# Kernel tuning notes

Hardware: AMD Instinct MI355X
Metric: run time of the kernel (lower is better)

Reference implementation:

```python
import jax, jax.numpy as jnp
import numpy as np

OUT_GRID = (256, 256)  # output_grid_shape


def setup_inputs() -> dict:
    key = jax.random.key(0)
    k1, k2 = jax.random.split(key)
    N, H, W, C = 16, 256, 256, 32
    x = jax.random.normal(k1, (N, H, W, C), dtype=jnp.float32)
    # loc network: global mean pool -> dense(6); small weights + identity-affine bias
    W_loc = jax.random.normal(k2, (C, 6), dtype=jnp.float32) * 0.01
    b_loc = jnp.array([1.0, 0.0, 0.0, 0.0, 1.0, 0.0], dtype=jnp.float32)
    return {"x": x, "W_loc": W_loc, "b_loc": b_loc}


def _spatial_transform(x, W_loc, b_loc):
    N, H, W, C = x.shape
    Ho, Wo = OUT_GRID
    # loc_network: params (N, 6) -> theta (N, 2, 3)
    params = jnp.mean(x, axis=(1, 2)) @ W_loc + b_loc
    theta = params.reshape(N, 2, 3)
    # grid_transform_fn: affine on [-1,1]-normalized output index grid
    gy = jnp.linspace(-1.0, 1.0, Ho, dtype=jnp.float32)
    gx = jnp.linspace(-1.0, 1.0, Wo, dtype=jnp.float32)
    Gy, Gx = jnp.meshgrid(gy, gx, indexing="ij")
    grid = jnp.stack([Gy.ravel(), Gx.ravel(), jnp.ones(Ho * Wo, jnp.float32)], axis=0)  # (3, Ho*Wo)
    coords = jnp.einsum("npq,qm->npm", theta, grid).reshape(N, 2, Ho, Wo)  # in ~[-1,1]
    # interpolate_bilinear with clip (wrap=False)
    maxes = jnp.array([H - 1, W - 1], dtype=jnp.float32)
    up = (coords + 1.0) * maxes[None, :, None, None] * 0.5  # upscale to pixel coords
    f = jnp.floor(up)
    frac = up - f  # (N, 2, Ho, Wo)
    fi = f.astype(jnp.int32)
    batch = jnp.arange(N)[:, None, None]
    out = jnp.zeros((N, Ho, Wo, C), dtype=x.dtype)
    for by in (0, 1):  # 2^dim corner offsets (bitfield)
        for bx in (0, 1):
            cy = jnp.clip(fi[:, 0] + by, 0, H - 1)
            cx = jnp.clip(fi[:, 1] + bx, 0, W - 1)
            wy = frac[:, 0] if by else 1.0 - frac[:, 0]
            wx = frac[:, 1] if bx else 1.0 - frac[:, 1]
            out = out + x[batch, cy, cx] * (wy * wx)[..., None]
    return out


def reference(x, W_loc, b_loc):
    return _spatial_transform(x, W_loc, b_loc)
```

## Files before the change

kernel.cpp:

```cpp
#include <hip/hip_runtime.h>


#define NIMG 16
#define HDIM 256
#define WDIM 256
#define CH   32
#define HW   (HDIM * WDIM)
#define BPI  64

typedef float f32x4 __attribute__((ext_vector_type(4)));

__global__ __launch_bounds__(256) void st_sum_kernel(
    const float* __restrict__ x, float* __restrict__ partials) {
    const int n   = blockIdx.x >> 6;
    const int blk = blockIdx.x & (BPI - 1);
    const int tid = threadIdx.x;
    const int cg  = tid & 7;
    const int sp  = tid >> 3;

    const float4* xp = (const float4*)(x + (size_t)n * HW * CH);
    float4 a0 = make_float4(0.f, 0.f, 0.f, 0.f);
    float4 a1 = make_float4(0.f, 0.f, 0.f, 0.f);
    float4 a2 = make_float4(0.f, 0.f, 0.f, 0.f);
    float4 a3 = make_float4(0.f, 0.f, 0.f, 0.f);
    int s = blk * 32 + sp;
    #pragma unroll
    for (int it = 0; it < 8; ++it) {
        float4 v0 = xp[(size_t)(s       ) * 8 + cg];
        float4 v1 = xp[(size_t)(s + 2048) * 8 + cg];
        float4 v2 = xp[(size_t)(s + 4096) * 8 + cg];
        float4 v3 = xp[(size_t)(s + 6144) * 8 + cg];
        a0.x += v0.x; a0.y += v0.y; a0.z += v0.z; a0.w += v0.w;
        a1.x += v1.x; a1.y += v1.y; a1.z += v1.z; a1.w += v1.w;
        a2.x += v2.x; a2.y += v2.y; a2.z += v2.z; a2.w += v2.w;
        a3.x += v3.x; a3.y += v3.y; a3.z += v3.z; a3.w += v3.w;
        s += 8192;
    }
    a0.x += a1.x; a0.y += a1.y; a0.z += a1.z; a0.w += a1.w;
    a2.x += a3.x; a2.y += a3.y; a2.z += a3.z; a2.w += a3.w;
    a0.x += a2.x; a0.y += a2.y; a0.z += a2.z; a0.w += a2.w;

    __shared__ float4 red[256];
    red[tid] = a0;
    __syncthreads();
    for (int stride = 16; stride >= 1; stride >>= 1) {
        if (sp < stride) {
            float4 o = red[(sp + stride) * 8 + cg];
            a0.x += o.x; a0.y += o.y; a0.z += o.z; a0.w += o.w;
            red[tid] = a0;
        }
        __syncthreads();
    }
    if (sp == 0) {
        ((float4*)(partials + ((size_t)blk * NIMG + n) * CH))[cg] = a0;
    }
}

__global__ __launch_bounds__(256) void st_interp_kernel(
    const float* __restrict__ x, const float* __restrict__ partials,
    const float* __restrict__ W_loc, const float* __restrict__ b_loc,
    float* __restrict__ out) {
    const int bid = (int)blockIdx.x;
    const int swz = (bid & 7) * 1024 + (bid >> 3);
    const int n   = swz >> 9;
    const int r   = swz & 511;
    const int tid = threadIdx.x;

    __shared__ float red2[8][CH];
    __shared__ float th_s[8];
    {
        const int c = tid & 31, g = tid >> 5;
        float s = 0.f;
        #pragma unroll
        for (int j = 0; j < 8; ++j)
            s += partials[(size_t)((g * 8 + j) * NIMG + n) * CH + c];
        red2[g][c] = s;
        __syncthreads();
        if (g == 0) {
            float m = 0.f;
            #pragma unroll
            for (int j = 0; j < 8; ++j) m += red2[j][c];
            red2[0][c] = m * (1.0f / (float)HW);
        }
        __syncthreads();
        if (tid < 6) {
            float acc = b_loc[tid];
            for (int c2 = 0; c2 < CH; ++c2)
                acc = fmaf(red2[0][c2], W_loc[c2 * 6 + tid], acc);
            th_s[tid] = acc;
        }
        __syncthreads();
    }
    const float t00 = th_s[0], t01 = th_s[1], t02 = th_s[2];
    const float t10 = th_s[3], t11 = th_s[4], t12 = th_s[5];

    const int ty = r >> 3;
    const int tx = r & 7;
    const int p  = tid >> 3;
    const int cg = tid & 7;

    const int ho = ty * 4 + (p >> 3);
    const float gy = fmaf((float)ho, 2.0f / 255.0f, -1.0f);
    const float cy = fmaf(t00, gy, t02);
    const float cx = fmaf(t10, gy, t12);

    const float4* xp = (const float4*)(x + (size_t)n * HW * CH);

    int   off0[4], off1[4], off2[4], off3[4];
    float w00[4], w01[4], w10[4], w11[4];
    int   wo[4];
    #pragma unroll
    for (int k = 0; k < 4; ++k) {
        wo[k] = tx * 32 + (p & 7) + k * 8;
        const float gx = fmaf((float)wo[k], 2.0f / 255.0f, -1.0f);
        const float uy = (fmaf(t01, gx, cy) + 1.0f) * 127.5f;
        const float ux = (fmaf(t11, gx, cx) + 1.0f) * 127.5f;
        const float fy = floorf(uy), fx = floorf(ux);
        const float ry = uy - fy, rx = ux - fx;
        const int iy0 = min(max((int)fy,     0), HDIM - 1);
        const int iy1 = min(max((int)fy + 1, 0), HDIM - 1);
        const int ix0 = min(max((int)fx,     0), WDIM - 1);
        const int ix1 = min(max((int)fx + 1, 0), WDIM - 1);
        off0[k] = (iy0 * WDIM + ix0) * 8;
        off1[k] = (iy0 * WDIM + ix1) * 8;
        off2[k] = (iy1 * WDIM + ix0) * 8;
        off3[k] = (iy1 * WDIM + ix1) * 8;
        w00[k] = (1.0f - ry) * (1.0f - rx);
        w01[k] = (1.0f - ry) * rx;
        w10[k] = ry * (1.0f - rx);
        w11[k] = ry * rx;
    }

    float4 v00[4], v01[4], v10[4], v11[4];
    #pragma unroll
    for (int k = 0; k < 4; ++k) {
        v00[k] = xp[(size_t)off0[k] + cg];
        v01[k] = xp[(size_t)off1[k] + cg];
        v10[k] = xp[(size_t)off2[k] + cg];
        v11[k] = xp[(size_t)off3[k] + cg];
    }

    f32x4* op = (f32x4*)(out + (size_t)n * HW * CH);
    #pragma unroll
    for (int k = 0; k < 4; ++k) {
        f32x4 o;
        o.x = v00[k].x * w00[k] + v01[k].x * w01[k] + v10[k].x * w10[k] + v11[k].x * w11[k];
        o.y = v00[k].y * w00[k] + v01[k].y * w01[k] + v10[k].y * w10[k] + v11[k].y * w11[k];
        o.z = v00[k].z * w00[k] + v01[k].z * w01[k] + v10[k].z * w10[k] + v11[k].z * w11[k];
        o.w = v00[k].w * w00[k] + v01[k].w * w01[k] + v10[k].w * w10[k] + v11[k].w * w11[k];
        __builtin_nontemporal_store(o, &op[(size_t)(ho * WDIM + wo[k]) * 8 + cg]);
    }
}

extern "C" void kernel_launch(void* const* d_in, const int* in_sizes, int n_in,
                              void* d_out, int out_size, void* d_ws, size_t ws_size,
                              hipStream_t stream) {
    const float* x     = (const float*)d_in[0];
    const float* W_loc = (const float*)d_in[1];
    const float* b_loc = (const float*)d_in[2];
    float* out = (float*)d_out;

    float* partials = (float*)d_ws;

    st_sum_kernel<<<NIMG * BPI, 256, 0, stream>>>(x, partials);
    st_interp_kernel<<<NIMG * (HW / 128), 256, 0, stream>>>(
        x, partials, W_loc, b_loc, out);
}
```

Baseline: 63.03 us.

## Stage bilinear source footprint in LDS per 8x32 output tile

The interpolation kernel now covers an 8x32 output tile per block instead of 4x32, which halves the grid. Each block computes the bounding box of its source footprint from the tile corners and, if that box fits within 384 pixels, copies it cooperatively into shared memory. The four corner gathers are then served from LDS rather than from scattered global loads, with a global-gather fallback when the box does not fit. The cost is 48KB of LDS per block, which lowers occupancy, plus an extra barrier and a serial row-by-row staging loop.

New measurement: 75.60 us. 1.2x slower.

```diff
diff --git a/kernel.cpp b/kernel.cpp
--- a/kernel.cpp
+++ b/kernel.cpp
@@ -7,6 +7,7 @@
 #define CH   32
 #define HW   (HDIM * WDIM)
 #define BPI  64
+#define STAGE_PX 384
 
 typedef float f32x4 __attribute__((ext_vector_type(4)));
 
@@ -61,13 +62,15 @@
     const float* __restrict__ W_loc, const float* __restrict__ b_loc,
     float* __restrict__ out) {
     const int bid = (int)blockIdx.x;
-    const int swz = (bid & 7) * 1024 + (bid >> 3);
-    const int n   = swz >> 9;
-    const int r   = swz & 511;
+    const int swz = (bid & 7) * 512 + (bid >> 3);
+    const int n   = swz >> 8;
+    const int r   = swz & 255;
     const int tid = threadIdx.x;
 
-    __shared__ float red2[8][CH];
-    __shared__ float th_s[8];
+    __shared__ float  red2[8][CH];
+    __shared__ float  th_s[8];
+    __shared__ float4 stage[STAGE_PX * 8];
+
     {
         const int c = tid & 31, g = tid >> 5;
         float s = 0.f;
@@ -94,61 +97,110 @@
     const float t00 = th_s[0], t01 = th_s[1], t02 = th_s[2];
     const float t10 = th_s[3], t11 = th_s[4], t12 = th_s[5];
 
-    const int ty = r >> 3;
-    const int tx = r & 7;
+    const int ty = r >> 3, tx = r & 7;
+    const int row0 = ty * 8, col0 = tx * 32;
     const int p  = tid >> 3;
     const int cg = tid & 7;
-
-    const int ho = ty * 4 + (p >> 3);
-    const float gy = fmaf((float)ho, 2.0f / 255.0f, -1.0f);
-    const float cy = fmaf(t00, gy, t02);
-    const float cx = fmaf(t10, gy, t12);
+    const int wo = col0 + p;
+
+    const float gx  = fmaf((float)wo, 2.0f / 255.0f, -1.0f);
+    const float ayx = fmaf(t01, gx, t02);
+    const float axx = fmaf(t11, gx, t12);
+
+    const float gyA = fmaf((float)row0,        2.0f / 255.0f, -1.0f);
+    const float gyB = fmaf((float)(row0 + 7),  2.0f / 255.0f, -1.0f);
+    const float gxA = fmaf((float)col0,        2.0f / 255.0f, -1.0f);
+    const float gxB = fmaf((float)(col0 + 31), 2.0f / 255.0f, -1.0f);
+    const float uy1 = (fmaf(t00, gyA, fmaf(t01, gxA, t02)) + 1.0f) * 127.5f;
+    const float uy2 = (fmaf(t00, gyA, fmaf(t01, gxB, t02)) + 1.0f) * 127.5f;
+    const float uy3 = (fmaf(t00, gyB, fmaf(t01, gxA, t02)) + 1.0f) * 127.5f;
+    const float uy4 = (fmaf(t00, gyB, fmaf(t01, gxB, t02)) + 1.0f) * 127.5f;
+    const float ux1 = (fmaf(t10, gyA, fmaf(t11, gxA, t12)) + 1.0f) * 127.5f;
+    const float ux2 = (fmaf(t10, gyA, fmaf(t11, gxB, t12)) + 1.0f) * 127.5f;
+    const float ux3 = (fmaf(t10, gyB, fmaf(t11, gxA, t12)) + 1.0f) * 127.5f;
+    const float ux4 = (fmaf(t10, gyB, fmaf(t11, gxB, t12)) + 1.0f) * 127.5f;
+    const float uymin = fminf(fminf(uy1, uy2), fminf(uy3, uy4));
+    const float uymax = fmaxf(fmaxf(uy1, uy2), fmaxf(uy3, uy4));
+    const float uxmin = fminf(fminf(ux1, ux2), fminf(ux3, ux4));
+    const float uxmax = fmaxf(fmaxf(ux1, ux2), fmaxf(ux3, ux4));
+    const int iy_lo = min(max((int)floorf(uymin),     0), HDIM - 1);
+    const int iy_hi = min(max((int)floorf(uymax) + 1, 0), HDIM - 1);
+    const int ix_lo = min(max((int)floorf(uxmin),     0), WDIM - 1);
+    const int ix_hi = min(max((int)floorf(uxmax) + 1, 0), WDIM - 1);
+    const int Rr = iy_hi - iy_lo + 1;
+    const int Cc = ix_hi - ix_lo + 1;
+    const bool finite = (uymin == uymin) && (uymax == uymax) &&
+                        (uxmin == uxmin) && (uxmax == uxmax);
+    const bool fits = finite && Rr >= 1 && Cc >= 1 && (Rr * Cc) <= STAGE_PX;
 
     const float4* xp = (const float4*)(x + (size_t)n * HW * CH);
-
-    int   off0[4], off1[4], off2[4], off3[4];
-    float w00[4], w01[4], w10[4], w11[4];
-    int   wo[4];
-    #pragma unroll
-    for (int k = 0; k < 4; ++k) {
-        wo[k] = tx * 32 + (p & 7) + k * 8;
-        const float gx = fmaf((float)wo[k], 2.0f / 255.0f, -1.0f);
-        const float uy = (fmaf(t01, gx, cy) + 1.0f) * 127.5f;
-        const float ux = (fmaf(t11, gx, cx) + 1.0f) * 127.5f;
-        const float fy = floorf(uy), fx = floorf(ux);
-        const float ry = uy - fy, rx = ux - fx;
-        const int iy0 = min(max((int)fy,     0), HDIM - 1);
-        const int iy1 = min(max((int)fy + 1, 0), HDIM - 1);
-        const int ix0 = min(max((int)fx,     0), WDIM - 1);
-        const int ix1 = min(max((int)fx + 1, 0), WDIM - 1);
-        off0[k] = (iy0 * WDIM + ix0) * 8;
-        off1[k] = (iy0 * WDIM + ix1) * 8;
-        off2[k] = (iy1 * WDIM + ix0) * 8;
-        off3[k] = (iy1 * WDIM + ix1) * 8;
-        w00[k] = (1.0f - ry) * (1.0f - rx);
-        w01[k] = (1.0f - ry) * rx;
-        w10[k] = ry * (1.0f - rx);
-        w11[k] = ry * rx;
-    }
-
-    float4 v00[4], v01[4], v10[4], v11[4];
-    #pragma unroll
-    for (int k = 0; k < 4; ++k) {
-        v00[k] = xp[(size_t)off0[k] + cg];
-        v01[k] = xp[(size_t)off1[k] + cg];
-        v10[k] = xp[(size_t)off2[k] + cg];
-        v11[k] = xp[(size_t)off3[k] + cg];
-    }
-
     f32x4* op = (f32x4*)(out + (size_t)n * HW * CH);
-    #pragma unroll
-    for (int k = 0; k < 4; ++k) {
-        f32x4 o;
-        o.x = v00[k].x * w00[k] + v01[k].x * w01[k] + v10[k].x * w10[k] + v11[k].x * w11[k];
-        o.y = v00[k].y * w00[k] + v01[k].y * w01[k] + v10[k].y * w10[k] + v11[k].y * w11[k];
-        o.z = v00[k].z * w00[k] + v01[k].z * w01[k] + v10[k].z * w10[k] + v11[k].z * w11[k];
-        o.w = v00[k].w * w00[k] + v01[k].w * w01[k] + v10[k].w * w10[k] + v11[k].w * w11[k];
-        __builtin_nontemporal_store(o, &op[(size_t)(ho * WDIM + wo[k]) * 8 + cg]);
+
+    if (fits) {
+        const int C8 = Cc * 8;
+        for (int rr = 0; rr < Rr; ++rr) {
+            const float4* src = xp + ((size_t)((iy_lo + rr) * WDIM + ix_lo)) * 8;
+            float4* dst = stage + rr * C8;
+            for (int u = tid; u < C8; u += 256) dst[u] = src[u];
+        }
+        __syncthreads();
+
+        #pragma unroll
+        for (int k = 0; k < 8; ++k) {
+            const int ho = row0 + k;
+            const float gy = fmaf((float)ho, 2.0f / 255.0f, -1.0f);
+            const float uy = (fmaf(t00, gy, ayx) + 1.0f) * 127.5f;
+            const float ux = (fmaf(t10, gy, axx) + 1.0f) * 127.5f;
+            const float fy = floorf(uy), fx = floorf(ux);
+            const float ry = uy - fy, rx = ux - fx;
+            const int iy0 = min(max((int)fy,     0), HDIM - 1);
+            const int iy1 = min(max((int)fy + 1, 0), HDIM - 1);
+            const int ix0 = min(max((int)fx,     0), WDIM - 1);
+            const int ix1 = min(max((int)fx + 1, 0), WDIM - 1);
+            const int ly0 = iy0 - iy_lo, ly1 = iy1 - iy_lo;
+            const int lx0 = ix0 - ix_lo, lx1 = ix1 - ix_lo;
+            float4 v00 = stage[(ly0 * Cc + lx0) * 8 + cg];
+            float4 v01 = stage[(ly0 * Cc + lx1) * 8 + cg];
+            float4 v10 = stage[(ly1 * Cc + lx0) * 8 + cg];
+            float4 v11 = stage[(ly1 * Cc + lx1) * 8 + cg];
+            const float w00 = (1.0f - ry) * (1.0f - rx);
+            const float w01 = (1.0f - ry) * rx;
+            const float w10 = ry * (1.0f - rx);
+            const float w11 = ry * rx;
+            f32x4 o;
+            o.x = v00.x * w00 + v01.x * w01 + v10.x * w10 + v11.x * w11;
+            o.y = v00.y * w00 + v01.y * w01 + v10.y * w10 + v11.y * w11;
+            o.z = v00.z * w00 + v01.z * w01 + v10.z * w10 + v11.z * w11;
+            o.w = v00.w * w00 + v01.w * w01 + v10.w * w10 + v11.w * w11;
+            __builtin_nontemporal_store(o, &op[(size_t)(ho * WDIM + wo) * 8 + cg]);
+        }
+    } else {
+        for (int k = 0; k < 8; ++k) {
+            const int ho = row0 + k;
+            const float gy = fmaf((float)ho, 2.0f / 255.0f, -1.0f);
+            const float uy = (fmaf(t00, gy, ayx) + 1.0f) * 127.5f;
+            const float ux = (fmaf(t10, gy, axx) + 1.0f) * 127.5f;
+            const float fy = floorf(uy), fx = floorf(ux);
+            const float ry = uy - fy, rx = ux - fx;
+            const int iy0 = min(max((int)fy,     0), HDIM - 1);
+            const int iy1 = min(max((int)fy + 1, 0), HDIM - 1);
+            const int ix0 = min(max((int)fx,     0), WDIM - 1);
+            const int ix1 = min(max((int)fx + 1, 0), WDIM - 1);
+            float4 v00 = xp[(size_t)(iy0 * WDIM + ix0) * 8 + cg];
+            float4 v01 = xp[(size_t)(iy0 * WDIM + ix1) * 8 + cg];
+            float4 v10 = xp[(size_t)(iy1 * WDIM + ix0) * 8 + cg];
+            float4 v11 = xp[(size_t)(iy1 * WDIM + ix1) * 8 + cg];
+            const float w00 = (1.0f - ry) * (1.0f - rx);
+            const float w01 = (1.0f - ry) * rx;
+            const float w10 = ry * (1.0f - rx);
+            const float w11 = ry * rx;
+            f32x4 o;
+            o.x = v00.x * w00 + v01.x * w01 + v10.x * w10 + v11.x * w11;
+            o.y = v00.y * w00 + v01.y * w01 + v10.y * w10 + v11.y * w11;
+            o.z = v00.z * w00 + v01.z * w01 + v10.z * w10 + v11.z * w11;
+            o.w = v00.w * w00 + v01.w * w01 + v10.w * w10 + v11.w * w11;
+            __builtin_nontemporal_store(o, &op[(size_t)(ho * WDIM + wo) * 8 + cg]);
+        }
     }
 }
 
@@ -163,6 +215,6 @@
     float* partials = (float*)d_ws;
 
     st_sum_kernel<<<NIMG * BPI, 256, 0, stream>>>(x, partials);
-    st_interp_kernel<<<NIMG * (HW / 128), 256, 0, stream>>>(
+    st_interp_kernel<<<NIMG * (HW / 256), 256, 0, stream>>>(
         x, partials, W_loc, b_loc, out);
 }
```

## Walk output rows per thread and reuse bottom-row corners as next top-row corners

Applied to the files above, without the earlier changes.

Each thread now produces 8 consecutive output rows at one column instead of 4 columns in one row. Because theta is near identity, the bottom corner pair of one row usually becomes the top pair of the next, so those two loads are skipped when the indices match. This roughly halves gather load instructions and halves the grid size. The cost is that loads now sit inside a serial dependent loop with a data-dependent branch, which may reduce memory-level parallelism, and each block also runs the theta reduction prologue over twice as much work.

Result: slower. 65.54 us (+4.0%).

```diff
diff --git a/kernel.cpp b/kernel.cpp
--- a/kernel.cpp
+++ b/kernel.cpp
@@ -61,9 +61,9 @@
     const float* __restrict__ W_loc, const float* __restrict__ b_loc,
     float* __restrict__ out) {
     const int bid = (int)blockIdx.x;
-    const int swz = (bid & 7) * 1024 + (bid >> 3);
-    const int n   = swz >> 9;
-    const int r   = swz & 511;
+    const int swz = (bid & 7) * 512 + (bid >> 3);
+    const int n   = swz >> 8;
+    const int r   = swz & 255;
     const int tid = threadIdx.x;
 
     __shared__ float red2[8][CH];
@@ -94,61 +94,56 @@
     const float t00 = th_s[0], t01 = th_s[1], t02 = th_s[2];
     const float t10 = th_s[3], t11 = th_s[4], t12 = th_s[5];
 
-    const int ty = r >> 3;
-    const int tx = r & 7;
+    const int ty = r >> 3, tx = r & 7;
     const int p  = tid >> 3;
     const int cg = tid & 7;
+    const int wo  = tx * 32 + p;
+    const int ho0 = ty * 8;
 
-    const int ho = ty * 4 + (p >> 3);
-    const float gy = fmaf((float)ho, 2.0f / 255.0f, -1.0f);
-    const float cy = fmaf(t00, gy, t02);
-    const float cx = fmaf(t10, gy, t12);
+    const float gx  = fmaf((float)wo, 2.0f / 255.0f, -1.0f);
+    const float ayx = fmaf(t01, gx, t02);
+    const float axx = fmaf(t11, gx, t12);
 
     const float4* xp = (const float4*)(x + (size_t)n * HW * CH);
+    f32x4* op = (f32x4*)(out + (size_t)n * HW * CH);
 
-    int   off0[4], off1[4], off2[4], off3[4];
-    float w00[4], w01[4], w10[4], w11[4];
-    int   wo[4];
+    float4 p0, p1;
+    int piy = -1, pix0 = -1, pix1 = -1;
+
     #pragma unroll
-    for (int k = 0; k < 4; ++k) {
-        wo[k] = tx * 32 + (p & 7) + k * 8;
-        const float gx = fmaf((float)wo[k], 2.0f / 255.0f, -1.0f);
-        const float uy = (fmaf(t01, gx, cy) + 1.0f) * 127.5f;
-        const float ux = (fmaf(t11, gx, cx) + 1.0f) * 127.5f;
+    for (int k = 0; k < 8; ++k) {
+        const int ho = ho0 + k;
+        const float gy = fmaf((float)ho, 2.0f / 255.0f, -1.0f);
+        const float uy = (fmaf(t00, gy, ayx) + 1.0f) * 127.5f;
+        const float ux = (fmaf(t10, gy, axx) + 1.0f) * 127.5f;
         const float fy = floorf(uy), fx = floorf(ux);
         const float ry = uy - fy, rx = ux - fx;
         const int iy0 = min(max((int)fy,     0), HDIM - 1);
         const int iy1 = min(max((int)fy + 1, 0), HDIM - 1);
         const int ix0 = min(max((int)fx,     0), WDIM - 1);
         const int ix1 = min(max((int)fx + 1, 0), WDIM - 1);
-        off0[k] = (iy0 * WDIM + ix0) * 8;
-        off1[k] = (iy0 * WDIM + ix1) * 8;
-        off2[k] = (iy1 * WDIM + ix0) * 8;
-        off3[k] = (iy1 * WDIM + ix1) * 8;
-        w00[k] = (1.0f - ry) * (1.0f - rx);
-        w01[k] = (1.0f - ry) * rx;
-        w10[k] = ry * (1.0f - rx);
-        w11[k] = ry * rx;
-    }
 
-    float4 v00[4], v01[4], v10[4], v11[4];
-    #pragma unroll
-    for (int k = 0; k < 4; ++k) {
-        v00[k] = xp[(size_t)off0[k] + cg];
-        v01[k] = xp[(size_t)off1[k] + cg];
-        v10[k] = xp[(size_t)off2[k] + cg];
-        v11[k] = xp[(size_t)off3[k] + cg];
-    }
+        if (k == 0 || !(iy0 == piy && ix0 == pix0 && ix1 == pix1)) {
+            p0 = xp[(size_t)(iy0 * WDIM + ix0) * 8 + cg];
+            p1 = xp[(size_t)(iy0 * WDIM + ix1) * 8 + cg];
+        }
+        const float4 c0 = xp[(size_t)(iy1 * WDIM + ix0) * 8 + cg];
+        const float4 c1 = xp[(size_t)(iy1 * WDIM + ix1) * 8 + cg];
 
-    f32x4* op = (f32x4*)(out + (size_t)n * HW * CH);
-    #pragma unroll
-    for (int k = 0; k < 4; ++k) {
+        const float w00 = (1.0f - ry) * (1.0f - rx);
+        const float w01 = (1.0f - ry) * rx;
+        const float w10 = ry * (1.0f - rx);
+        const float w11 = ry * rx;
+
         f32x4 o;
-        o.x = v00[k].x * w00[k] + v01[k].x * w01[k] + v10[k].x * w10[k] + v11[k].x * w11[k];
-        o.y = v00[k].y * w00[k] + v01[k].y * w01[k] + v10[k].y * w10[k] + v11[k].y * w11[k];
-        o.z = v00[k].z * w00[k] + v01[k].z * w01[k] + v10[k].z * w10[k] + v11[k].z * w11[k];
-        o.w = v00[k].w * w00[k] + v01[k].w * w01[k] + v10[k].w * w10[k] + v11[k].w * w11[k];
-        __builtin_nontemporal_store(o, &op[(size_t)(ho * WDIM + wo[k]) * 8 + cg]);
+        o.x = p0.x * w00 + p1.x * w01 + c0.x * w10 + c1.x * w11;
+        o.y = p0.y * w00 + p1.y * w01 + c0.y * w10 + c1.y * w11;
+        o.z = p0.z * w00 + p1.z * w01 + c0.z * w10 + c1.z * w11;
+        o.w = p0.w * w00 + p1.w * w01 + c0.w * w10 + c1.w * w11;
+        __builtin_nontemporal_store(o, &op[(size_t)(ho * WDIM + wo) * 8 + cg]);
+
+        p0 = c0; p1 = c1;
+        piy = iy1; pix0 = ix0; pix1 = ix1;
     }
 }
 
@@ -163,6 +158,6 @@
     float* partials = (float*)d_ws;
 
     st_sum_kernel<<<NIMG * BPI, 256, 0, stream>>>(x, partials);
-    st_interp_kernel<<<NIMG * (HW / 128), 256, 0, stream>>>(
+    st_interp_kernel<<<NIMG * (HW / 256), 256, 0, stream>>>(
         x, partials, W_loc, b_loc, out);
 }
```
